# Performance work log

Measured on AMD Instinct MI355X. Metric: run time of the kernel, lower is better.

The kernel has to match this reference:

```python
import jax, jax.numpy as jnp
import numpy as np

DIM = 2048
HID = 1024
E = 16
TOP_K = 2
S_SHARED = 2


def setup_inputs() -> dict:
    key = jax.random.key(0)
    ks = jax.random.split(key, 6)
    scale = 0.02
    x = jax.random.normal(ks[0], (2, 2048, DIM), dtype=jnp.float32)
    gate_w = jax.random.normal(ks[1], (DIM, E), dtype=jnp.float32) * scale
    shared_w1 = jax.random.normal(ks[2], (S_SHARED, DIM, HID), dtype=jnp.float32) * scale
    shared_w2 = jax.random.normal(ks[3], (S_SHARED, HID, DIM), dtype=jnp.float32) * scale
    w1 = jax.random.normal(ks[4], (E, DIM, HID), dtype=jnp.float32) * scale
    w2 = jax.random.normal(ks[5], (E, HID, DIM), dtype=jnp.float32) * scale
    return {"x": x, "gate_w": gate_w, "shared_w1": shared_w1,
            "shared_w2": shared_w2, "w1": w1, "w2": w2}


def reference(x, gate_w, shared_w1, shared_w2, w1, w2):
    orig_shape = x.shape
    xf = x.reshape(-1, orig_shape[-1])  # [T, D]

    # Shared experts: sum of SiLU MLPs
    hs = jax.nn.silu(jnp.einsum('td,sdh->sth', xf, shared_w1))
    shared_out = jnp.einsum('sth,shd->td', hs, shared_w2)

    # Gating
    probs = jax.nn.softmax(xf @ gate_w, axis=-1)              # [T, E]
    weights, indices = jax.lax.top_k(probs, TOP_K)            # [T, K]
    weights = weights / weights.sum(axis=-1, keepdims=True)
    aux_loss = (probs.mean(axis=0) ** 2).sum() * E

    # Combine weights per (token, expert): top_k indices are distinct
    combine = (jax.nn.one_hot(indices, E, dtype=xf.dtype) *
               weights[..., None]).sum(axis=1)                # [T, E]

    # Dense all-expert compute (reference form of gather-GEMM-scatter)
    h = jax.nn.silu(jnp.einsum('td,edh->eth', xf, w1))        # [E, T, H]
    y = jnp.einsum('eth,ehd->etd', h, w2)                     # [E, T, D]
    routed_out = jnp.einsum('te,etd->td', combine, y)         # [T, D]

    out = (shared_out + routed_out).reshape(orig_shape)
    return out, aux_loss
```

## Files before the change

kernel.cpp:

```cpp
#include <hip/hip_runtime.h>
#include <math.h>

typedef unsigned short u16;
typedef __bf16 bf16x8 __attribute__((ext_vector_type(8)));
typedef float f32x4 __attribute__((ext_vector_type(4)));

#define T_TOK 4096
#define DIMD 2048
#define HIDD 1024
#define NEXP 16
#define RMAX 10240
#define MAXBLK 96
#define BM 128
#define BN 128
#define BK 32

__device__ __forceinline__ u16 f2b(float f) {
  unsigned u = __builtin_bit_cast(unsigned, f);
  unsigned r = (u + 0x7FFFu + ((u >> 16) & 1u)) >> 16;
  return (u16)r;
}

__device__ __forceinline__ void gld16(const void* g, void* l) {
  __builtin_amdgcn_global_load_lds(
      (const __attribute__((address_space(1))) void*)g,
      (__attribute__((address_space(3))) void*)l, 16, 0, 0);
}


__global__ void k_zero(float* __restrict__ o) {
  const int i = blockIdx.x * blockDim.x + threadIdx.x;
  float4 z = {0.f, 0.f, 0.f, 0.f};
  ((float4*)o)[i] = z;
}

__global__ void k_init(int* perm, int* cnt, int* fill) {
  int i = blockIdx.x * blockDim.x + threadIdx.x;
  if (i < RMAX) perm[i] = -1;
  if (i < NEXP) { cnt[i] = 0; fill[i] = 0; }
}

__global__ void k_cvt(const float* __restrict__ x, u16* __restrict__ xb) {
  const int i = blockIdx.x * blockDim.x + threadIdx.x;
  const float4 v = ((const float4*)x)[i];
  union { u16 u[4]; unsigned long long q; } t;
  t.u[0] = f2b(v.x); t.u[1] = f2b(v.y); t.u[2] = f2b(v.z); t.u[3] = f2b(v.w);
  ((unsigned long long*)xb)[i] = t.q;
}

__global__ __launch_bounds__(256)
void k_tr(const float* __restrict__ W, u16* __restrict__ Wt,
          int K, int N, long estride, int ld_out) {
  __shared__ float t[64][65];
  const int e = blockIdx.z;
  const float* Win = W + (size_t)e * (size_t)K * (size_t)N;
  u16* Wo = Wt + (size_t)e * (size_t)estride;
  const int n0 = blockIdx.x * 64, k0 = blockIdx.y * 64;
  const int r = threadIdx.x >> 4;
  const int c = (threadIdx.x & 15) * 4;
#pragma unroll
  for (int p = 0; p < 4; ++p) {
    const int kk = p * 16 + r;
    const float4 v = *(const float4*)&Win[(size_t)(k0 + kk) * N + n0 + c];
    t[kk][c] = v.x; t[kk][c + 1] = v.y; t[kk][c + 2] = v.z; t[kk][c + 3] = v.w;
  }
  __syncthreads();
#pragma unroll
  for (int p = 0; p < 4; ++p) {
    const int nn = p * 16 + r;
    ushort4 o;
    o.x = f2b(t[c + 0][nn]); o.y = f2b(t[c + 1][nn]);
    o.z = f2b(t[c + 2][nn]); o.w = f2b(t[c + 3][nn]);
    *(ushort4*)&Wo[(size_t)(n0 + nn) * ld_out + k0 + c] = o;
  }
}

__global__ __launch_bounds__(256)
void k_gate(const float* __restrict__ x, const float* __restrict__ gw,
            int* __restrict__ top2i, float* __restrict__ top2w,
            int* __restrict__ cnt, float* __restrict__ partial) {
  const int e = threadIdx.x & 15;
  const int tt = threadIdx.x >> 4;
  const int t = blockIdx.x * 16 + tt;
  const float* xp = x + (size_t)t * DIMD;
  float acc = 0.f;
#pragma unroll 8
  for (int k = 0; k < DIMD; ++k) acc = fmaf(xp[k], gw[k * NEXP + e], acc);
  __shared__ float lg[16][17];
  __shared__ float pr[16][17];
  lg[tt][e] = acc;
  __syncthreads();
  if (e == 0) {
    float l[16];
    float mx = -1e30f;
    for (int j = 0; j < 16; ++j) { l[j] = lg[tt][j]; mx = fmaxf(mx, l[j]); }
    float s = 0.f;
    for (int j = 0; j < 16; ++j) { l[j] = expf(l[j] - mx); s += l[j]; }
    const float inv = 1.f / s;
    float p1 = -1.f, p2 = -1.f; int i1 = 0, i2 = 0;
    for (int j = 0; j < 16; ++j) {
      const float p = l[j] * inv;
      pr[tt][j] = p;
      if (p > p1) { p2 = p1; i2 = i1; p1 = p; i1 = j; }
      else if (p > p2) { p2 = p; i2 = j; }
    }
    const float wsum = p1 + p2;
    top2i[t * 2 + 0] = i1;
    top2i[t * 2 + 1] = i2;
    top2w[t * 2 + 0] = p1 / wsum;
    top2w[t * 2 + 1] = p2 / wsum;
    atomicAdd(&cnt[i1], 1);
    atomicAdd(&cnt[i2], 1);
  }
  __syncthreads();
  if (tt == 0) {
    float s = 0.f;
    for (int j = 0; j < 16; ++j) s += pr[j][e];
    partial[blockIdx.x * 16 + e] = s;
  }
}

__global__ __launch_bounds__(256)
void k_aux(const float* __restrict__ partial, float* __restrict__ auxOut) {
  __shared__ float s[16][17];
  const int e = threadIdx.x & 15, c = threadIdx.x >> 4;
  float a = 0.f;
  for (int b = c; b < 256; b += 16) a += partial[b * 16 + e];
  s[c][e] = a;
  __syncthreads();
  if (threadIdx.x == 0) {
    float aux = 0.f;
    for (int j = 0; j < 16; ++j) {
      float tot = 0.f;
      for (int cc = 0; cc < 16; ++cc) tot += s[cc][j];
      const float m = tot / (float)T_TOK;
      aux += m * m;
    }
    auxOut[0] = aux * (float)NEXP;
  }
}

__global__ void k_off(const int* __restrict__ cnt, int* __restrict__ offs,
                      int* __restrict__ tbl_e, int* __restrict__ tbl_r0,
                      int* __restrict__ nblk) {
  if (threadIdx.x != 0 || blockIdx.x != 0) return;
  int o = 0, nb = 0;
  for (int e = 0; e < NEXP; ++e) {
    offs[e] = o;
    const int b = (cnt[e] + BM - 1) / BM;
    for (int i = 0; i < b; ++i) { tbl_e[nb] = e; tbl_r0[nb] = o + i * BM; ++nb; }
    o += b * BM;
  }
  offs[NEXP] = o;
  nblk[0] = nb;
}

__global__ void k_fill(const int* __restrict__ top2i, const float* __restrict__ top2w,
                       const int* __restrict__ offs, int* __restrict__ fill,
                       int* __restrict__ perm, float* __restrict__ wrow) {
  const int id = blockIdx.x * blockDim.x + threadIdx.x;
  if (id >= T_TOK * 2) return;
  const int e = top2i[id];
  const int pos = atomicAdd(&fill[e], 1);
  const int r = offs[e] + pos;
  perm[r] = id >> 1;
  wrow[r] = top2w[id];
}

__device__ __forceinline__ void gemm_core(
    const u16* __restrict__ ap0, const u16* __restrict__ ap1,
    const u16* __restrict__ bp0, const u16* __restrict__ bp1, int K,
    u16* lA0, u16* lA1, u16* lB0, u16* lB1,
    const u16* aRd, const u16* bRd, f32x4 (&acc)[4][4]) {
  for (int k0 = 0; k0 < K; k0 += BK) {
    gld16(ap0 + k0, lA0);
    gld16(ap1 + k0, lA1);
    gld16(bp0 + k0, lB0);
    gld16(bp1 + k0, lB1);
    __syncthreads();
    bf16x8 af[4], bq[4];
#pragma unroll
    for (int i = 0; i < 4; ++i) af[i] = *(const bf16x8*)(aRd + i * 16 * BK);
#pragma unroll
    for (int j = 0; j < 4; ++j) bq[j] = *(const bf16x8*)(bRd + j * 16 * BK);
#pragma unroll
    for (int i = 0; i < 4; ++i)
#pragma unroll
      for (int j = 0; j < 4; ++j)
        acc[i][j] = __builtin_amdgcn_mfma_f32_16x16x32_bf16(af[i], bq[j], acc[i][j], 0, 0, 0);
    __syncthreads();
  }
}

__global__ __launch_bounds__(256)
void k_up(const u16* __restrict__ xb, const u16* __restrict__ sw1t,
          const u16* __restrict__ w1t, u16* __restrict__ hbS,
          u16* __restrict__ hbR, const int* __restrict__ perm,
          const int* __restrict__ tbl_e, const int* __restrict__ tbl_r0,
          const int* __restrict__ nblk) {
  __shared__ u16 As[BM * BK];
  __shared__ u16 Bs[BN * BK];

  const int bx = blockIdx.x, by = blockIdx.y;
  const int tid = threadIdx.x;
  const int w = tid >> 6, lane = tid & 63;
  const int lr = lane >> 2;
  const int lk = (lane & 3) * 8;

  const bool routed = bx >= 64;
  int expert, r0, ra0, ra1;
  const u16* B;
  if (!routed) {
    expert = bx >> 5;
    r0 = (bx & 31) * BM;
    B = sw1t + (size_t)expert * (size_t)HIDD * DIMD;
    ra0 = r0 + w * 32 + lr; ra1 = ra0 + 16;
  } else {
    const int rbx = bx - 64;
    if (rbx >= *nblk) return;
    expert = tbl_e[rbx];
    r0 = tbl_r0[rbx];
    B = w1t + (size_t)expert * (size_t)HIDD * DIMD;
    const int rr0 = r0 + w * 32 + lr, rr1 = rr0 + 16;
    const int p0 = perm[rr0]; ra0 = (p0 < 0) ? 0 : p0;
    const int p1 = perm[rr1]; ra1 = (p1 < 0) ? 0 : p1;
  }

  const int n0 = by * BN;
  const u16* ap0 = xb + (size_t)ra0 * DIMD + lk;
  const u16* ap1 = xb + (size_t)ra1 * DIMD + lk;
  const u16* bp0 = B + (size_t)(n0 + w * 32 + lr) * DIMD + lk;
  const u16* bp1 = bp0 + (size_t)16 * DIMD;
  u16* lA0 = &As[w * 1024];
  u16* lA1 = &As[w * 1024 + 512];
  u16* lB0 = &Bs[w * 1024];
  u16* lB1 = &Bs[w * 1024 + 512];

  f32x4 acc[4][4];
#pragma unroll
  for (int i = 0; i < 4; ++i)
#pragma unroll
    for (int j = 0; j < 4; ++j) {
      acc[i][j][0] = 0.f; acc[i][j][1] = 0.f; acc[i][j][2] = 0.f; acc[i][j][3] = 0.f;
    }

  const int wr = (w >> 1) * 64, wc = (w & 1) * 64;
  const int lm = lane & 15, lq = lane >> 4;
  const u16* aRd = &As[(wr + lm) * BK + lq * 8];
  const u16* bRd = &Bs[(wc + lm) * BK + lq * 8];

  gemm_core(ap0, ap1, bp0, bp1, DIMD, lA0, lA1, lB0, lB1, aRd, bRd, acc);

#pragma unroll
  for (int i = 0; i < 4; ++i) {
#pragma unroll
    for (int r = 0; r < 4; ++r) {
      const int row = r0 + wr + i * 16 + lq * 4 + r;
      u16* dst = routed ? &hbR[(size_t)row * HIDD]
                        : &hbS[(size_t)row * DIMD + expert * HIDD];
#pragma unroll
      for (int j = 0; j < 4; ++j) {
        const int gc = n0 + wc + j * 16 + lm;
        const float v = acc[i][j][r];
        const float s = v / (1.f + expf(-v));
        dst[gc] = f2b(s);
      }
    }
  }
}

__global__ __launch_bounds__(256)
void k_down(const u16* __restrict__ hbS, const u16* __restrict__ hbR,
            const u16* __restrict__ sw2ct, const u16* __restrict__ w2t,
            float* __restrict__ out, const int* __restrict__ perm,
            const float* __restrict__ wrow,
            const int* __restrict__ tbl_e, const int* __restrict__ tbl_r0,
            const int* __restrict__ nblk) {
  __shared__ u16 As[BM * BK];
  __shared__ u16 Bs[BN * BK];

  const int bx = blockIdx.x, by = blockIdx.y;
  const int tid = threadIdx.x;
  const int w = tid >> 6, lane = tid & 63;
  const int lr = lane >> 2;
  const int lk = (lane & 3) * 8;

  const bool routed = bx >= 32;
  int r0, K, ld;
  const u16 *Amat, *B;
  if (!routed) {
    r0 = bx * BM;
    Amat = hbS; K = DIMD; ld = DIMD;
    B = sw2ct;
  } else {
    const int rbx = bx - 32;
    if (rbx >= *nblk) return;
    const int expert = tbl_e[rbx];
    r0 = tbl_r0[rbx];
    Amat = hbR; K = HIDD; ld = HIDD;
    B = w2t + (size_t)expert * (size_t)DIMD * HIDD;
  }

  const int n0 = by * BN;
  const u16* ap0 = Amat + (size_t)(r0 + w * 32 + lr) * ld + lk;
  const u16* ap1 = ap0 + (size_t)16 * ld;
  const u16* bp0 = B + (size_t)(n0 + w * 32 + lr) * ld + lk;
  const u16* bp1 = bp0 + (size_t)16 * ld;
  u16* lA0 = &As[w * 1024];
  u16* lA1 = &As[w * 1024 + 512];
  u16* lB0 = &Bs[w * 1024];
  u16* lB1 = &Bs[w * 1024 + 512];

  f32x4 acc[4][4];
#pragma unroll
  for (int i = 0; i < 4; ++i)
#pragma unroll
    for (int j = 0; j < 4; ++j) {
      acc[i][j][0] = 0.f; acc[i][j][1] = 0.f; acc[i][j][2] = 0.f; acc[i][j][3] = 0.f;
    }

  const int wr = (w >> 1) * 64, wc = (w & 1) * 64;
  const int lm = lane & 15, lq = lane >> 4;
  const u16* aRd = &As[(wr + lm) * BK + lq * 8];
  const u16* bRd = &Bs[(wc + lm) * BK + lq * 8];

  gemm_core(ap0, ap1, bp0, bp1, K, lA0, lA1, lB0, lB1, aRd, bRd, acc);

#pragma unroll
  for (int i = 0; i < 4; ++i) {
#pragma unroll
    for (int r = 0; r < 4; ++r) {
      const int rr = r0 + wr + i * 16 + lq * 4 + r;
      int t; float wt;
      if (!routed) { t = rr; wt = 1.f; }
      else { t = perm[rr]; wt = (t >= 0) ? wrow[rr] : 0.f; }
      if (t >= 0) {
        float* dst = &out[(size_t)t * DIMD];
#pragma unroll
        for (int j = 0; j < 4; ++j) {
          const int gc = n0 + wc + j * 16 + lm;
          atomicAdd(&dst[gc], wt * acc[i][j][r]);
        }
      }
    }
  }
}


extern "C" void kernel_launch(void* const* d_in, const int* in_sizes, int n_in,
                              void* d_out, int out_size, void* d_ws, size_t ws_size,
                              hipStream_t stream) {
  const float* x   = (const float*)d_in[0];
  const float* gw  = (const float*)d_in[1];
  const float* sw1 = (const float*)d_in[2];
  const float* sw2 = (const float*)d_in[3];
  const float* w1  = (const float*)d_in[4];
  const float* w2  = (const float*)d_in[5];
  float* out = (float*)d_out;

  char* ws = (char*)d_ws;
  u16* xb    = (u16*)(ws);
  u16* hbS   = (u16*)(ws + (size_t)( 16 << 20));
  u16* hbR   = (u16*)(ws + (size_t)( 32 << 20));
  u16* sw1t  = (u16*)(ws + (size_t)( 52 << 20));
  u16* sw2ct = (u16*)(ws + (size_t)( 60 << 20));
  u16* w1t   = (u16*)(ws + (size_t)( 68 << 20));
  u16* w2t   = (u16*)(ws + (size_t)(132 << 20));
  char* p = ws + (size_t)(196 << 20);
  int*   top2i   = (int*)p;    p += T_TOK * 2 * 4;
  float* top2w   = (float*)p;  p += T_TOK * 2 * 4;
  int*   perm    = (int*)p;    p += RMAX * 4;
  float* wrow    = (float*)p;  p += RMAX * 4;
  int*   cnt     = (int*)p;    p += 16 * 4;
  int*   fill    = (int*)p;    p += 16 * 4;
  int*   offs    = (int*)p;    p += 32 * 4;
  int*   tbl_e   = (int*)p;    p += MAXBLK * 4;
  int*   tbl_r0  = (int*)p;    p += MAXBLK * 4;
  int*   nblk    = (int*)p;    p += 16 * 4;
  float* partial = (float*)p;  p += 256 * 16 * 4;

  k_zero<<<(T_TOK * DIMD / 4) / 256, 256, 0, stream>>>(out);
  k_init<<<(RMAX + 255) / 256, 256, 0, stream>>>(perm, cnt, fill);
  k_cvt<<<(T_TOK * DIMD / 4) / 256, 256, 0, stream>>>(x, xb);
  k_gate<<<T_TOK / 16, 256, 0, stream>>>(x, gw, top2i, top2w, cnt, partial);
  k_off<<<1, 64, 0, stream>>>(cnt, offs, tbl_e, tbl_r0, nblk);
  k_fill<<<(T_TOK * 2 + 255) / 256, 256, 0, stream>>>(top2i, top2w, offs, fill, perm, wrow);
  k_aux<<<1, 256, 0, stream>>>(partial, out + (size_t)T_TOK * DIMD);

  k_tr<<<dim3(1024 / 64, 2048 / 64,  2), 256, 0, stream>>>(sw1, sw1t, 2048, 1024, 1024l * 2048, 2048);
  k_tr<<<dim3(2048 / 64, 1024 / 64,  2), 256, 0, stream>>>(sw2, sw2ct, 1024, 2048, 1024, 2048);
  k_tr<<<dim3(1024 / 64, 2048 / 64, 16), 256, 0, stream>>>(w1, w1t, 2048, 1024, 1024l * 2048, 2048);
  k_tr<<<dim3(2048 / 64, 1024 / 64, 16), 256, 0, stream>>>(w2, w2t, 1024, 2048, 2048l * 1024, 1024);

  k_up<<<dim3(64 + 80, 8), 256, 0, stream>>>(xb, sw1t, w1t, hbS, hbR,
                                             perm, tbl_e, tbl_r0, nblk);
  k_down<<<dim3(32 + 80, 16), 256, 0, stream>>>(hbS, hbR, sw2ct, w2t, out,
                                                perm, wrow, tbl_e, tbl_r0, nblk);
}
```

Baseline: 826.0 us.

## Double-buffer LDS in expert GEMMs and grow tiles to 256 rows with 8 waves

Replaces the single-buffered load/sync/compute loop with an LDS double buffer, so the global-to-LDS loads for the next K slice are issued before the MFMAs on the current slice, leaving one barrier per step. Row tiles grow from 128 to 256 and blocks from 4 to 8 waves. Grid sizes, routed padding capacity and workspace offsets are adjusted to match, which halves the block count and raises padding waste per expert. Larger LDS footprint and 512-thread blocks may lower occupancy.

New measurement: 834.1 us. About the same (+1.0%).

```diff
diff --git a/kernel.cpp b/kernel.cpp
--- a/kernel.cpp
+++ b/kernel.cpp
@@ -9,9 +9,9 @@
 #define DIMD 2048
 #define HIDD 1024
 #define NEXP 16
-#define RMAX 10240
+#define RMAX 12288
 #define MAXBLK 96
-#define BM 128
+#define BM 256
 #define BN 128
 #define BK 32
 
@@ -167,39 +167,71 @@
   wrow[r] = top2w[id];
 }
 
-__device__ __forceinline__ void gemm_core(
+__device__ __forceinline__ void gemm_body(
     const u16* __restrict__ ap0, const u16* __restrict__ ap1,
-    const u16* __restrict__ bp0, const u16* __restrict__ bp1, int K,
-    u16* lA0, u16* lA1, u16* lB0, u16* lB1,
-    const u16* aRd, const u16* bRd, f32x4 (&acc)[4][4]) {
-  for (int k0 = 0; k0 < K; k0 += BK) {
-    gld16(ap0 + k0, lA0);
-    gld16(ap1 + k0, lA1);
-    gld16(bp0 + k0, lB0);
-    gld16(bp1 + k0, lB1);
-    __syncthreads();
+    const u16* __restrict__ bp0, int K,
+    u16* __restrict__ As, u16* __restrict__ Bs,
+    int w, int lane, f32x4 (&acc)[4][4]) {
+  const int aoff_st = w * 16 * BK;
+  const int boff_st = w * 16 * BK;
+  const int wm = w >> 1, wn = w & 1;
+  const int lm = lane & 15, lq = lane >> 4;
+  const int aoff_rd = (wm * 64 + lm) * BK + lq * 8;
+  const int boff_rd = (wn * 64 + lm) * BK + lq * 8;
+  const int nst = K / BK;
+
+  gld16(ap0, As + aoff_st);
+  gld16(ap1, As + 128 * BK + aoff_st);
+  gld16(bp0, Bs + boff_st);
+  __syncthreads();
+
+  int cur = 0;
+  for (int t = 1; t < nst; ++t) {
+    const int k1 = t * BK;
+    u16* dA = As + (cur ^ 1) * (BM * BK) + aoff_st;
+    gld16(ap0 + k1, dA);
+    gld16(ap1 + k1, dA + 128 * BK);
+    gld16(bp0 + k1, Bs + (cur ^ 1) * (BN * BK) + boff_st);
+
+    const u16* aR = As + cur * (BM * BK) + aoff_rd;
+    const u16* bR = Bs + cur * (BN * BK) + boff_rd;
     bf16x8 af[4], bq[4];
 #pragma unroll
-    for (int i = 0; i < 4; ++i) af[i] = *(const bf16x8*)(aRd + i * 16 * BK);
-#pragma unroll
-    for (int j = 0; j < 4; ++j) bq[j] = *(const bf16x8*)(bRd + j * 16 * BK);
+    for (int i = 0; i < 4; ++i) af[i] = *(const bf16x8*)(aR + i * 16 * BK);
+#pragma unroll
+    for (int j = 0; j < 4; ++j) bq[j] = *(const bf16x8*)(bR + j * 16 * BK);
 #pragma unroll
     for (int i = 0; i < 4; ++i)
 #pragma unroll
       for (int j = 0; j < 4; ++j)
         acc[i][j] = __builtin_amdgcn_mfma_f32_16x16x32_bf16(af[i], bq[j], acc[i][j], 0, 0, 0);
     __syncthreads();
-  }
-}
-
-__global__ __launch_bounds__(256)
+    cur ^= 1;
+  }
+  {
+    const u16* aR = As + cur * (BM * BK) + aoff_rd;
+    const u16* bR = Bs + cur * (BN * BK) + boff_rd;
+    bf16x8 af[4], bq[4];
+#pragma unroll
+    for (int i = 0; i < 4; ++i) af[i] = *(const bf16x8*)(aR + i * 16 * BK);
+#pragma unroll
+    for (int j = 0; j < 4; ++j) bq[j] = *(const bf16x8*)(bR + j * 16 * BK);
+#pragma unroll
+    for (int i = 0; i < 4; ++i)
+#pragma unroll
+      for (int j = 0; j < 4; ++j)
+        acc[i][j] = __builtin_amdgcn_mfma_f32_16x16x32_bf16(af[i], bq[j], acc[i][j], 0, 0, 0);
+  }
+}
+
+__global__ __launch_bounds__(512, 4)
 void k_up(const u16* __restrict__ xb, const u16* __restrict__ sw1t,
           const u16* __restrict__ w1t, u16* __restrict__ hbS,
           u16* __restrict__ hbR, const int* __restrict__ perm,
           const int* __restrict__ tbl_e, const int* __restrict__ tbl_r0,
           const int* __restrict__ nblk) {
-  __shared__ u16 As[BM * BK];
-  __shared__ u16 Bs[BN * BK];
+  __shared__ u16 As[2 * BM * BK];
+  __shared__ u16 Bs[2 * BN * BK];
 
   const int bx = blockIdx.x, by = blockIdx.y;
   const int tid = threadIdx.x;
@@ -207,34 +239,29 @@
   const int lr = lane >> 2;
   const int lk = (lane & 3) * 8;
 
-  const bool routed = bx >= 64;
-  int expert, r0, ra0, ra1;
+  const bool routed = bx >= 32;
+  int expert, r0, ga0, ga1;
   const u16* B;
   if (!routed) {
-    expert = bx >> 5;
-    r0 = (bx & 31) * BM;
+    expert = bx >> 4;
+    r0 = (bx & 15) * BM;
     B = sw1t + (size_t)expert * (size_t)HIDD * DIMD;
-    ra0 = r0 + w * 32 + lr; ra1 = ra0 + 16;
+    ga0 = r0 + w * 16 + lr;
+    ga1 = r0 + 128 + w * 16 + lr;
   } else {
-    const int rbx = bx - 64;
+    const int rbx = bx - 32;
     if (rbx >= *nblk) return;
     expert = tbl_e[rbx];
     r0 = tbl_r0[rbx];
     B = w1t + (size_t)expert * (size_t)HIDD * DIMD;
-    const int rr0 = r0 + w * 32 + lr, rr1 = rr0 + 16;
-    const int p0 = perm[rr0]; ra0 = (p0 < 0) ? 0 : p0;
-    const int p1 = perm[rr1]; ra1 = (p1 < 0) ? 0 : p1;
+    const int p0 = perm[r0 + w * 16 + lr];       ga0 = (p0 < 0) ? 0 : p0;
+    const int p1 = perm[r0 + 128 + w * 16 + lr]; ga1 = (p1 < 0) ? 0 : p1;
   }
 
   const int n0 = by * BN;
-  const u16* ap0 = xb + (size_t)ra0 * DIMD + lk;
-  const u16* ap1 = xb + (size_t)ra1 * DIMD + lk;
-  const u16* bp0 = B + (size_t)(n0 + w * 32 + lr) * DIMD + lk;
-  const u16* bp1 = bp0 + (size_t)16 * DIMD;
-  u16* lA0 = &As[w * 1024];
-  u16* lA1 = &As[w * 1024 + 512];
-  u16* lB0 = &Bs[w * 1024];
-  u16* lB1 = &Bs[w * 1024 + 512];
+  const u16* ap0 = xb + (size_t)ga0 * DIMD + lk;
+  const u16* ap1 = xb + (size_t)ga1 * DIMD + lk;
+  const u16* bp0 = B + (size_t)(n0 + w * 16 + lr) * DIMD + lk;
 
   f32x4 acc[4][4];
 #pragma unroll
@@ -244,23 +271,20 @@
       acc[i][j][0] = 0.f; acc[i][j][1] = 0.f; acc[i][j][2] = 0.f; acc[i][j][3] = 0.f;
     }
 
-  const int wr = (w >> 1) * 64, wc = (w & 1) * 64;
+  gemm_body(ap0, ap1, bp0, DIMD, As, Bs, w, lane, acc);
+
+  const int wm = w >> 1, wn = w & 1;
   const int lm = lane & 15, lq = lane >> 4;
-  const u16* aRd = &As[(wr + lm) * BK + lq * 8];
-  const u16* bRd = &Bs[(wc + lm) * BK + lq * 8];
-
-  gemm_core(ap0, ap1, bp0, bp1, DIMD, lA0, lA1, lB0, lB1, aRd, bRd, acc);
-
 #pragma unroll
   for (int i = 0; i < 4; ++i) {
 #pragma unroll
     for (int r = 0; r < 4; ++r) {
-      const int row = r0 + wr + i * 16 + lq * 4 + r;
+      const int row = r0 + wm * 64 + i * 16 + lq * 4 + r;
       u16* dst = routed ? &hbR[(size_t)row * HIDD]
                         : &hbS[(size_t)row * DIMD + expert * HIDD];
 #pragma unroll
       for (int j = 0; j < 4; ++j) {
-        const int gc = n0 + wc + j * 16 + lm;
+        const int gc = n0 + wn * 64 + j * 16 + lm;
         const float v = acc[i][j][r];
         const float s = v / (1.f + expf(-v));
         dst[gc] = f2b(s);
@@ -269,15 +293,15 @@
   }
 }
 
-__global__ __launch_bounds__(256)
+__global__ __launch_bounds__(512, 4)
 void k_down(const u16* __restrict__ hbS, const u16* __restrict__ hbR,
             const u16* __restrict__ sw2ct, const u16* __restrict__ w2t,
             float* __restrict__ out, const int* __restrict__ perm,
             const float* __restrict__ wrow,
             const int* __restrict__ tbl_e, const int* __restrict__ tbl_r0,
             const int* __restrict__ nblk) {
-  __shared__ u16 As[BM * BK];
-  __shared__ u16 Bs[BN * BK];
+  __shared__ u16 As[2 * BM * BK];
+  __shared__ u16 Bs[2 * BN * BK];
 
   const int bx = blockIdx.x, by = blockIdx.y;
   const int tid = threadIdx.x;
@@ -285,7 +309,7 @@
   const int lr = lane >> 2;
   const int lk = (lane & 3) * 8;
 
-  const bool routed = bx >= 32;
+  const bool routed = bx >= 16;
   int r0, K, ld;
   const u16 *Amat, *B;
   if (!routed) {
@@ -293,7 +317,7 @@
     Amat = hbS; K = DIMD; ld = DIMD;
     B = sw2ct;
   } else {
-    const int rbx = bx - 32;
+    const int rbx = bx - 16;
     if (rbx >= *nblk) return;
     const int expert = tbl_e[rbx];
     r0 = tbl_r0[rbx];
@@ -302,14 +326,9 @@
   }
 
   const int n0 = by * BN;
-  const u16* ap0 = Amat + (size_t)(r0 + w * 32 + lr) * ld + lk;
-  const u16* ap1 = ap0 + (size_t)16 * ld;
-  const u16* bp0 = B + (size_t)(n0 + w * 32 + lr) * ld + lk;
-  const u16* bp1 = bp0 + (size_t)16 * ld;
-  u16* lA0 = &As[w * 1024];
-  u16* lA1 = &As[w * 1024 + 512];
-  u16* lB0 = &Bs[w * 1024];
-  u16* lB1 = &Bs[w * 1024 + 512];
+  const u16* ap0 = Amat + (size_t)(r0 + w * 16 + lr) * ld + lk;
+  const u16* ap1 = Amat + (size_t)(r0 + 128 + w * 16 + lr) * ld + lk;
+  const u16* bp0 = B + (size_t)(n0 + w * 16 + lr) * ld + lk;
 
   f32x4 acc[4][4];
 #pragma unroll
@@ -319,18 +338,15 @@
       acc[i][j][0] = 0.f; acc[i][j][1] = 0.f; acc[i][j][2] = 0.f; acc[i][j][3] = 0.f;
     }
 
-  const int wr = (w >> 1) * 64, wc = (w & 1) * 64;
+  gemm_body(ap0, ap1, bp0, K, As, Bs, w, lane, acc);
+
+  const int wm = w >> 1, wn = w & 1;
   const int lm = lane & 15, lq = lane >> 4;
-  const u16* aRd = &As[(wr + lm) * BK + lq * 8];
-  const u16* bRd = &Bs[(wc + lm) * BK + lq * 8];
-
-  gemm_core(ap0, ap1, bp0, bp1, K, lA0, lA1, lB0, lB1, aRd, bRd, acc);
-
 #pragma unroll
   for (int i = 0; i < 4; ++i) {
 #pragma unroll
     for (int r = 0; r < 4; ++r) {
-      const int rr = r0 + wr + i * 16 + lq * 4 + r;
+      const int rr = r0 + wm * 64 + i * 16 + lq * 4 + r;
       int t; float wt;
       if (!routed) { t = rr; wt = 1.f; }
       else { t = perm[rr]; wt = (t >= 0) ? wrow[rr] : 0.f; }
@@ -338,7 +354,7 @@
         float* dst = &out[(size_t)t * DIMD];
 #pragma unroll
         for (int j = 0; j < 4; ++j) {
-          const int gc = n0 + wc + j * 16 + lm;
+          const int gc = n0 + wn * 64 + j * 16 + lm;
           atomicAdd(&dst[gc], wt * acc[i][j][r]);
         }
       }
@@ -362,11 +378,11 @@
   u16* xb    = (u16*)(ws);
   u16* hbS   = (u16*)(ws + (size_t)( 16 << 20));
   u16* hbR   = (u16*)(ws + (size_t)( 32 << 20));
-  u16* sw1t  = (u16*)(ws + (size_t)( 52 << 20));
-  u16* sw2ct = (u16*)(ws + (size_t)( 60 << 20));
-  u16* w1t   = (u16*)(ws + (size_t)( 68 << 20));
-  u16* w2t   = (u16*)(ws + (size_t)(132 << 20));
-  char* p = ws + (size_t)(196 << 20);
+  u16* sw1t  = (u16*)(ws + (size_t)( 56 << 20));
+  u16* sw2ct = (u16*)(ws + (size_t)( 64 << 20));
+  u16* w1t   = (u16*)(ws + (size_t)( 72 << 20));
+  u16* w2t   = (u16*)(ws + (size_t)(136 << 20));
+  char* p = ws + (size_t)(200 << 20);
   int*   top2i   = (int*)p;    p += T_TOK * 2 * 4;
   float* top2w   = (float*)p;  p += T_TOK * 2 * 4;
   int*   perm    = (int*)p;    p += RMAX * 4;
@@ -392,8 +408,8 @@
   k_tr<<<dim3(1024 / 64, 2048 / 64, 16), 256, 0, stream>>>(w1, w1t, 2048, 1024, 1024l * 2048, 2048);
   k_tr<<<dim3(2048 / 64, 1024 / 64, 16), 256, 0, stream>>>(w2, w2t, 1024, 2048, 2048l * 1024, 1024);
 
-  k_up<<<dim3(64 + 80, 8), 256, 0, stream>>>(xb, sw1t, w1t, hbS, hbR,
+  k_up<<<dim3(32 + 48, 8), 512, 0, stream>>>(xb, sw1t, w1t, hbS, hbR,
                                              perm, tbl_e, tbl_r0, nblk);
-  k_down<<<dim3(32 + 80, 16), 256, 0, stream>>>(hbS, hbR, sw2ct, w2t, out,
+  k_down<<<dim3(16 + 48, 16), 512, 0, stream>>>(hbS, hbR, sw2ct, w2t, out,
                                                 perm, wrow, tbl_e, tbl_r0, nblk);
 }
```
